# Performance work log

Measured on AMD Instinct MI355X. Metric: run time of the kernel, lower is better.

The kernel has to match this reference:

```python
import jax, jax.numpy as jnp
import numpy as np

N_NODES = 50000
N_EDGES = 800000
LATENT = 128
N_CENTERS = 100

def shifted_softplus(x):
    # softplus(x) - log(2), the standard (G)SchNet activation
    return jax.nn.softplus(x) - jnp.log(2.0).astype(x.dtype)

def setup_inputs() -> dict:
    key = jax.random.key(0)
    k_n, k_s, k_r, k_w1, k_w2 = jax.random.split(key, 5)
    nodes = jax.random.normal(k_n, (N_NODES, 3), dtype=jnp.float32) * 3.0  # 3D positions
    senders = jax.random.randint(k_s, (N_EDGES,), 0, N_NODES)
    receivers = jax.random.randint(k_r, (N_EDGES,), 0, N_NODES)
    # hk.nets.MLP default truncated-normal init ~ 1/sqrt(fan_in)
    W1 = jax.random.normal(k_w1, (N_CENTERS, LATENT), dtype=jnp.float32) / np.sqrt(N_CENTERS)
    b1 = jnp.zeros((LATENT,), dtype=jnp.float32)
    W2 = jax.random.normal(k_w2, (LATENT, LATENT), dtype=jnp.float32) / np.sqrt(LATENT)
    b2 = jnp.zeros((LATENT,), dtype=jnp.float32)
    return {"nodes": nodes, "senders": senders, "receivers": receivers,
            "W1": W1, "b1": b1, "W2": W2, "b2": b2}

def reference(nodes, senders, receivers, W1, b1, W2, b2):
    # Gather endpoint positions per edge and compute scalar distance
    diff = nodes[senders] - nodes[receivers]            # [E, 3]
    dist = jnp.linalg.norm(diff, axis=-1)               # [E]
    # Gaussian RBF embedding: 100 centers in [0, 10], gamma = 1.0
    centers = jnp.linspace(0.0, 10.0, N_CENTERS).astype(dist.dtype)  # [100]
    rbf = jnp.exp(-jnp.square(dist[:, None] - centers[None, :]))     # [E, 100]
    # 2-layer MLP: activation between layers only (activate_final=False)
    h = shifted_softplus(rbf @ W1 + b1)                 # [E, latent]
    out = h @ W2 + b2                                   # [E, latent]
    return out
```

## Files before the change

kernel.cpp:

```cpp
#include <hip/hip_runtime.h>
#include <hip/hip_fp16.h>
#include <math.h>


#define N_NODES_C   50000
#define N_EDGES_C   800000
#define LATENT_C    128
#define N_CENTERS_C 100
#define TABK        1024
#define DMAX        16.0f
#define LN2F        0.69314718056f

typedef float  v4f __attribute__((ext_vector_type(4)));
typedef _Float16 h4 __attribute__((ext_vector_type(4)));

__device__ __forceinline__ float shifted_softplus(float x) {
    return fmaxf(x, 0.0f) + log1pf(expf(-fabsf(x))) - LN2F;
}

__global__ void build_table_kernel(const float* __restrict__ W1, const float* __restrict__ b1,
                                   const float* __restrict__ W2, const float* __restrict__ b2,
                                   _Float16* __restrict__ table) {
    __shared__ float rbf[N_CENTERS_C];
    __shared__ float hbuf[LATENT_C];
    const int j = threadIdx.x;
    const float d = (float)blockIdx.x * (DMAX / (float)TABK);

    if (j < N_CENTERS_C) {
        const float c = (float)j * (10.0f / 99.0f);
        const float x = d - c;
        rbf[j] = expf(-x * x);
    }
    __syncthreads();

    float a = b1[j];
    #pragma unroll 4
    for (int c = 0; c < N_CENTERS_C; ++c)
        a = fmaf(rbf[c], W1[c * LATENT_C + j], a);
    hbuf[j] = shifted_softplus(a);
    __syncthreads();

    float o = b2[j];
    #pragma unroll 4
    for (int i = 0; i < LATENT_C; ++i)
        o = fmaf(hbuf[i], W2[i * LATENT_C + j], o);

    table[(size_t)blockIdx.x * LATENT_C + j] = (_Float16)o;
}

__global__ void edge_write_kernel(const float* __restrict__ nodes,
                                  const int* __restrict__ senders,
                                  const int* __restrict__ receivers,
                                  const _Float16* __restrict__ table,
                                  float* __restrict__ out) {
    const int lane = threadIdx.x & 63;
    const int half = lane >> 5;
    const int li   = lane & 31;
    const int wid  = (blockIdx.x * blockDim.x + threadIdx.x) >> 6;
    const int nw   = (gridDim.x * blockDim.x) >> 6;

    for (int base = wid * 4; base + 3 < N_EDGES_C; base += nw * 4) {
        const int e0 = base + half;
        const int e1 = base + 2 + half;

        const int s0 = senders[e0],  r0i = receivers[e0];
        const int s1 = senders[e1],  r1i = receivers[e1];

        const float dx0 = nodes[3 * s0 + 0] - nodes[3 * r0i + 0];
        const float dy0 = nodes[3 * s0 + 1] - nodes[3 * r0i + 1];
        const float dz0 = nodes[3 * s0 + 2] - nodes[3 * r0i + 2];
        const float dx1 = nodes[3 * s1 + 0] - nodes[3 * r1i + 0];
        const float dy1 = nodes[3 * s1 + 1] - nodes[3 * r1i + 1];
        const float dz1 = nodes[3 * s1 + 2] - nodes[3 * r1i + 2];

        const float dist0 = sqrtf(fmaf(dx0, dx0, fmaf(dy0, dy0, dz0 * dz0)));
        const float dist1 = sqrtf(fmaf(dx1, dx1, fmaf(dy1, dy1, dz1 * dz1)));

        const float t0 = fminf(dist0 * ((float)TABK / DMAX), (float)TABK - 0.5f);
        const float t1 = fminf(dist1 * ((float)TABK / DMAX), (float)TABK - 0.5f);
        const int   k0 = (int)t0;  const float f0 = t0 - (float)k0;
        const int   k1 = (int)t1;  const float f1 = t1 - (float)k1;

        const h4* p0 = (const h4*)(table + (size_t)k0 * LATENT_C);
        const h4* p1 = (const h4*)(table + (size_t)k1 * LATENT_C);
        const h4 a0 = p0[li], b0 = p0[li + 32];
        const h4 a1 = p1[li], b1 = p1[li + 32];

        v4f o0, o1;
        #pragma unroll
        for (int c = 0; c < 4; ++c) {
            const float A0 = (float)a0[c], B0 = (float)b0[c];
            const float A1 = (float)a1[c], B1 = (float)b1[c];
            o0[c] = fmaf(f0, B0 - A0, A0);
            o1[c] = fmaf(f1, B1 - A1, A1);
        }

        v4f* po0 = (v4f*)(out + (size_t)base * LATENT_C);
        v4f* po1 = (v4f*)(out + (size_t)(base + 2) * LATENT_C);
        __builtin_nontemporal_store(o0, &po0[lane]);
        __builtin_nontemporal_store(o1, &po1[lane]);
    }
}

__global__ void edge_direct_kernel(const float* __restrict__ nodes,
                                   const int* __restrict__ senders,
                                   const int* __restrict__ receivers,
                                   const float* __restrict__ W1, const float* __restrict__ b1,
                                   const float* __restrict__ W2, const float* __restrict__ b2,
                                   float* __restrict__ out) {
    __shared__ float rbf[N_CENTERS_C];
    __shared__ float hbuf[LATENT_C];
    const int j = threadIdx.x;

    for (int e = blockIdx.x; e < N_EDGES_C; e += gridDim.x) {
        const int s = senders[e];
        const int r = receivers[e];
        const float dx = nodes[3 * s + 0] - nodes[3 * r + 0];
        const float dy = nodes[3 * s + 1] - nodes[3 * r + 1];
        const float dz = nodes[3 * s + 2] - nodes[3 * r + 2];
        const float dist = sqrtf(fmaf(dx, dx, fmaf(dy, dy, dz * dz)));

        if (j < N_CENTERS_C) {
            const float c = (float)j * (10.0f / 99.0f);
            const float x = dist - c;
            rbf[j] = expf(-x * x);
        }
        __syncthreads();

        float a = b1[j];
        #pragma unroll 4
        for (int c = 0; c < N_CENTERS_C; ++c)
            a = fmaf(rbf[c], W1[c * LATENT_C + j], a);
        hbuf[j] = shifted_softplus(a);
        __syncthreads();

        float o = b2[j];
        #pragma unroll 4
        for (int i = 0; i < LATENT_C; ++i)
            o = fmaf(hbuf[i], W2[i * LATENT_C + j], o);
        out[(size_t)e * LATENT_C + j] = o;

        __syncthreads();
    }
}

extern "C" void kernel_launch(void* const* d_in, const int* in_sizes, int n_in,
                              void* d_out, int out_size, void* d_ws, size_t ws_size,
                              hipStream_t stream) {
    const float* nodes     = (const float*)d_in[0];
    const int*   senders   = (const int*)  d_in[1];
    const int*   receivers = (const int*)  d_in[2];
    const float* W1        = (const float*)d_in[3];
    const float* b1        = (const float*)d_in[4];
    const float* W2        = (const float*)d_in[5];
    const float* b2        = (const float*)d_in[6];
    float*       out       = (float*)d_out;

    const size_t table_bytes = (size_t)(TABK + 1) * LATENT_C * sizeof(_Float16);

    if (ws_size >= table_bytes) {
        _Float16* table = (_Float16*)d_ws;

        build_table_kernel<<<TABK + 1, LATENT_C, 0, stream>>>(W1, b1, W2, b2, table);
        edge_write_kernel<<<2048, 256, 0, stream>>>(nodes, senders, receivers, table, out);
    } else {
        edge_direct_kernel<<<16384, LATENT_C, 0, stream>>>(nodes, senders, receivers,
                                                           W1, b1, W2, b2, out);
    }
}
```

Before: 83.62 us.

## Compute per-edge distance once per lane and broadcast via wave shuffles

Each wave now owns a contiguous block of 64 edges. Every lane computes the distance for one edge with coalesced index loads, then the wave broadcasts table positions through __shfl while writing out four edges per iteration. Before, each lane redundantly reloaded the indices and node positions for the edges it wrote. The grid-stride loop is replaced by a fixed grid of 3125 blocks sized exactly to the edge count, which assumes N_EDGES divides evenly into 64-edge waves.

```diff
diff --git a/kernel.cpp b/kernel.cpp
--- a/kernel.cpp
+++ b/kernel.cpp
@@ -57,27 +57,22 @@
     const int half = lane >> 5;
     const int li   = lane & 31;
     const int wid  = (blockIdx.x * blockDim.x + threadIdx.x) >> 6;
-    const int nw   = (gridDim.x * blockDim.x) >> 6;
+    const int base = wid * 64;
 
-    for (int base = wid * 4; base + 3 < N_EDGES_C; base += nw * 4) {
-        const int e0 = base + half;
-        const int e1 = base + 2 + half;
+    const int e = base + lane;
+    const int s = senders[e];
+    const int r = receivers[e];
+    const float dx = nodes[3 * s + 0] - nodes[3 * r + 0];
+    const float dy = nodes[3 * s + 1] - nodes[3 * r + 1];
+    const float dz = nodes[3 * s + 2] - nodes[3 * r + 2];
+    const float dist = sqrtf(fmaf(dx, dx, fmaf(dy, dy, dz * dz)));
+    const float t = fminf(dist * ((float)TABK / DMAX), (float)TABK - 0.5f);
 
-        const int s0 = senders[e0],  r0i = receivers[e0];
-        const int s1 = senders[e1],  r1i = receivers[e1];
-
-        const float dx0 = nodes[3 * s0 + 0] - nodes[3 * r0i + 0];
-        const float dy0 = nodes[3 * s0 + 1] - nodes[3 * r0i + 1];
-        const float dz0 = nodes[3 * s0 + 2] - nodes[3 * r0i + 2];
-        const float dx1 = nodes[3 * s1 + 0] - nodes[3 * r1i + 0];
-        const float dy1 = nodes[3 * s1 + 1] - nodes[3 * r1i + 1];
-        const float dz1 = nodes[3 * s1 + 2] - nodes[3 * r1i + 2];
-
-        const float dist0 = sqrtf(fmaf(dx0, dx0, fmaf(dy0, dy0, dz0 * dz0)));
-        const float dist1 = sqrtf(fmaf(dx1, dx1, fmaf(dy1, dy1, dz1 * dz1)));
-
-        const float t0 = fminf(dist0 * ((float)TABK / DMAX), (float)TABK - 0.5f);
-        const float t1 = fminf(dist1 * ((float)TABK / DMAX), (float)TABK - 0.5f);
+    #pragma unroll 4
+    for (int i = 0; i < 16; ++i) {
+        const int eb = base + 4 * i;
+        const float t0 = __shfl(t, 4 * i + half, 64);
+        const float t1 = __shfl(t, 4 * i + 2 + half, 64);
         const int   k0 = (int)t0;  const float f0 = t0 - (float)k0;
         const int   k1 = (int)t1;  const float f1 = t1 - (float)k1;
 
@@ -95,8 +90,8 @@
             o1[c] = fmaf(f1, B1 - A1, A1);
         }
 
-        v4f* po0 = (v4f*)(out + (size_t)base * LATENT_C);
-        v4f* po1 = (v4f*)(out + (size_t)(base + 2) * LATENT_C);
+        v4f* po0 = (v4f*)(out + (size_t)eb * LATENT_C);
+        v4f* po1 = (v4f*)(out + (size_t)(eb + 2) * LATENT_C);
         __builtin_nontemporal_store(o0, &po0[lane]);
         __builtin_nontemporal_store(o1, &po1[lane]);
     }
@@ -162,7 +157,7 @@
         _Float16* table = (_Float16*)d_ws;
 
         build_table_kernel<<<TABK + 1, LATENT_C, 0, stream>>>(W1, b1, W2, b2, table);
-        edge_write_kernel<<<2048, 256, 0, stream>>>(nodes, senders, receivers, table, out);
+        edge_write_kernel<<<3125, 256, 0, stream>>>(nodes, senders, receivers, table, out);
     } else {
         edge_direct_kernel<<<16384, LATENT_C, 0, stream>>>(nodes, senders, receivers,
                                                            W1, b1, W2, b2, out);
```

After: 84.89 us. No clear change (+1.5%).
